# Kernel optimization log

Measured on AMD Instinct MI355X. Metric: run time of the kernel, lower is better.

The kernel has to match this reference:

```python
import jax, jax.numpy as jnp
import numpy as np

B, S, HID = 2, 2048, 4096
H, KV, D = 32, 8, 128
ROPE_BASE = 10000.0
SCALE = 1.0 / (D ** 0.5)


def setup_inputs() -> dict:
    key = jax.random.key(0)
    k1, k2, k3 = jax.random.split(key, 3)
    hidden_states = jax.random.normal(k1, (B, S, HID), dtype=jnp.float32)
    position_ids = jnp.broadcast_to(jnp.arange(S, dtype=jnp.int32)[None, :], (B, S))
    Wqkv = jax.random.normal(k2, ((H + 2 * KV) * D, HID), dtype=jnp.float32) * (HID ** -0.5)
    Wo = jax.random.normal(k3, (HID, HID), dtype=jnp.float32) * (HID ** -0.5)
    return {"hidden_states": hidden_states, "position_ids": position_ids,
            "Wqkv": Wqkv, "Wo": Wo}


def _rotate_half(x):
    x1, x2 = jnp.split(x, 2, axis=-1)
    return jnp.concatenate([-x2, x1], axis=-1)


def _rope_cos_sin(position_ids):
    # inv_freq: [D/2]
    inv_freq = 1.0 / (ROPE_BASE ** (jnp.arange(0, D, 2, dtype=jnp.float32) / D))
    freqs = position_ids.astype(jnp.float32)[:, :, None] * inv_freq[None, None, :]  # [B,S,D/2]
    emb = jnp.concatenate([freqs, freqs], axis=-1)  # [B,S,D]
    # broadcast over heads: [B,1,S,D]
    return jnp.cos(emb)[:, None, :, :], jnp.sin(emb)[:, None, :, :]


def reference(hidden_states, position_ids, Wqkv, Wo):
    # fused QKV projection (no bias)
    qkv = jnp.einsum('bsh,oh->bso', hidden_states, Wqkv)  # [B,S,(H+2KV)*D]
    q, k, v = jnp.split(qkv, [H * D, (H + KV) * D], axis=-1)
    q = q.reshape(B, S, H, D).transpose(0, 2, 1, 3)    # [B,H,S,D]
    k = k.reshape(B, S, KV, D).transpose(0, 2, 1, 3)   # [B,KV,S,D]
    v = v.reshape(B, S, KV, D).transpose(0, 2, 1, 3)   # [B,KV,S,D]

    cos, sin = _rope_cos_sin(position_ids)
    q = q * cos + _rotate_half(q) * sin
    k = k * cos + _rotate_half(k) * sin

    # GQA: repeat_interleave kv heads to match q heads
    rep = H // KV
    k_full = jnp.repeat(k, rep, axis=1)  # [B,H,S,D]
    v_full = jnp.repeat(v, rep, axis=1)

    scores = jnp.einsum('bhqd,bhkd->bhqk', q, k_full) * SCALE  # [B,H,S,S]
    causal = jnp.tril(jnp.ones((S, S), dtype=bool))
    scores = jnp.where(causal[None, None, :, :], scores, jnp.float32(-jnp.inf))
    attn = jax.nn.softmax(scores, axis=-1)
    out = jnp.einsum('bhqk,bhkd->bhqd', attn, v_full)  # [B,H,S,D]
    out = out.transpose(0, 2, 1, 3).reshape(B, S, H * D)
    return jnp.einsum('bso,ho->bsh', out, Wo)  # o_proj, Wo is [out,in]
```

## Files before the change

kernel.cpp:

```cpp
#include <hip/hip_runtime.h>
#include <stdint.h>
#include <stddef.h>

#define Bsz   2
#define Ssz   2048
#define HIDsz 4096
#define Hsz   32
#define KVsz  8
#define Dsz   128
#define NQKV  6144
#define QSCALE 0.12752057463f
#define L2_1E4_64 0.20762050595f

typedef __bf16 bf16x8 __attribute__((ext_vector_type(8)));
typedef __bf16 bf16x2 __attribute__((ext_vector_type(2)));
typedef float  f32x4  __attribute__((ext_vector_type(4)));
typedef float  f32x16 __attribute__((ext_vector_type(16)));
typedef unsigned short u16;
typedef u16 u16x4 __attribute__((ext_vector_type(4)));
typedef u16 u16x8 __attribute__((ext_vector_type(8)));
typedef uint32_t u32x4 __attribute__((ext_vector_type(4)));

__device__ __forceinline__ u16 f2bf(float f) {
  uint32_t u = __builtin_bit_cast(uint32_t, f);
  u = (u + 0x7FFFu + ((u >> 16) & 1u)) >> 16;
  return (u16)u;
}
__device__ __forceinline__ float bf2f(u16 h) {
  return __builtin_bit_cast(float, (uint32_t)h << 16);
}
__device__ __forceinline__ uint32_t packc(float lo, float hi_) {
  bf16x2 t;
  t[0] = (__bf16)lo; t[1] = (__bf16)hi_;
  return __builtin_bit_cast(uint32_t, t);
}

#define GLDS(gp, lp) __builtin_amdgcn_global_load_lds( \
    (__attribute__((address_space(1))) void*)(void*)(gp), \
    (__attribute__((address_space(3))) void*)(lp), 16, 0, 0)

#define N4_HS  ((Bsz * Ssz * HIDsz) / 4)
#define N4_WQ  ((NQKV * HIDsz) / 4)
#define N4_WO  ((HIDsz * HIDsz) / 4)
__global__ __launch_bounds__(256) void k_cvt3(const float* __restrict__ hs,
                                              const float* __restrict__ wqkv,
                                              const float* __restrict__ wo,
                                              u16* __restrict__ xbf,
                                              u16* __restrict__ wqbf,
                                              u16* __restrict__ wobf) {
  int i = blockIdx.x * 256 + threadIdx.x;
  const float* src; u16* dst; int off;
  if (i < N4_HS)                   { src = hs;   dst = xbf;  off = i; }
  else if (i < N4_HS + N4_WQ)      { src = wqkv; dst = wqbf; off = i - N4_HS; }
  else if (i < N4_HS + N4_WQ + N4_WO) { src = wo; dst = wobf; off = i - N4_HS - N4_WQ; }
  else return;
  float4 v = ((const float4*)src)[off];
  u16x4 o;
  o.x = f2bf(v.x); o.y = f2bf(v.y); o.z = f2bf(v.z); o.w = f2bf(v.w);
  ((u16x4*)dst)[off] = o;
}


#define BARX do { asm volatile("" ::: "memory"); __builtin_amdgcn_s_barrier(); \
                  asm volatile("" ::: "memory"); } while (0)
#define VM6  asm volatile("s_waitcnt vmcnt(6)" ::: "memory")
#define VM0  asm volatile("s_waitcnt vmcnt(0)" ::: "memory")

#define LOADA4(P_, Q_, F_) do {                                               \
    afr[F_][0] = LDA(P_, Q_, 0, 0); afr[F_][1] = LDA(P_, Q_, 0, 1);           \
    afr[F_][2] = LDA(P_, Q_, 1, 0); afr[F_][3] = LDA(P_, Q_, 1, 1);           \
  } while (0)

#define LOADB8(P_) do {                                                       \
    _Pragma("unroll") for (int nf = 0; nf < 4; ++nf) {                        \
      bfr[nf][0] = LDB(P_, nf, 0); bfr[nf][1] = LDB(P_, nf, 1); }             \
  } while (0)

#define MMA16(Q_, F_) do {                                                    \
    __builtin_amdgcn_s_setprio(1);                                            \
    _Pragma("unroll") for (int nf = 0; nf < 4; ++nf) {                        \
      acc[(Q_)*2][nf]   = __builtin_amdgcn_mfma_f32_16x16x32_bf16(afr[F_][0], bfr[nf][0], acc[(Q_)*2][nf],   0,0,0); \
      acc[(Q_)*2+1][nf] = __builtin_amdgcn_mfma_f32_16x16x32_bf16(afr[F_][2], bfr[nf][0], acc[(Q_)*2+1][nf], 0,0,0); \
    }                                                                         \
    _Pragma("unroll") for (int nf = 0; nf < 4; ++nf) {                        \
      acc[(Q_)*2][nf]   = __builtin_amdgcn_mfma_f32_16x16x32_bf16(afr[F_][1], bfr[nf][1], acc[(Q_)*2][nf],   0,0,0); \
      acc[(Q_)*2+1][nf] = __builtin_amdgcn_mfma_f32_16x16x32_bf16(afr[F_][3], bfr[nf][1], acc[(Q_)*2+1][nf], 0,0,0); \
    }                                                                         \
    __builtin_amdgcn_s_setprio(0);                                            \
  } while (0)

#define TLS 258

template <int MODE>
__global__ __launch_bounds__(512, 1) void k_gemm256(const u16* __restrict__ A,
                                                    const u16* __restrict__ Bm,
                                                    float* __restrict__ Cv,
                                                    const int* __restrict__ pos,
                                                    u16* __restrict__ Qr,
                                                    u16* __restrict__ Kr,
                                                    u16* __restrict__ Vt,
                                                    int M, int N, int K) {
  constexpr int LDS_BYTES = MODE ? (256 * TLS * 2) : (4 * 256 * 64 * 2);
  __shared__ __align__(16) char LDSBUF[LDS_BYTES];
  u16* SA0 = (u16*)LDSBUF;
  u16* SB0 = (u16*)(LDSBUF + 65536);
  const int tid = threadIdx.x;
  const int w = tid >> 6, lane = tid & 63;
  const int g = lane >> 4, t = lane & 15;
  const int wr = w >> 2, wc = w & 3;
  const int MBt = M >> 8;
  const int cpx = gridDim.x >> 3;
  const int swz = (blockIdx.x & 7) * cpx + (blockIdx.x >> 3);
  const int bm = swz % MBt, bn = swz / MBt;
  const int m0 = bm << 8, n0 = bn << 8;

  const char* Ab = (const char*)A;
  const char* Bb = (const char*)Bm;
  const size_t rowK = (size_t)K * 2;
  const int srcx = ((lane & 7) ^ (lane >> 3)) << 4;
  const int l3 = lane >> 3;
  const int tx = (t & 7) << 4;

  auto SToff = [&](int h, int j) -> int {
    int ii = w * 2 + j;
    return (ii < 8) ? (h * 64 + ii * 8) : (128 + h * 64 + (ii - 8) * 8);
  };
  auto STAGE_A = [&](int p, int T, int h) {
#pragma unroll
    for (int j = 0; j < 2; ++j) {
      int rb = SToff(h, j);
      GLDS(Ab + (size_t)(m0 + rb + l3) * rowK + (size_t)T * 128 + srcx,
           &SA0[p * 16384 + rb * 64]);
    }
  };
  auto STAGE_B = [&](int p, int T, int h) {
#pragma unroll
    for (int j = 0; j < 2; ++j) {
      int rb = SToff(h, j);
      GLDS(Bb + (size_t)(n0 + rb + l3) * rowK + (size_t)T * 128 + srcx,
           &SB0[p * 16384 + rb * 64]);
    }
  };
  auto LDA = [&](int p, int q, int fr, int kk) -> bf16x8 {
    int ar = wr * 128 + q * 32 + fr * 16 + t;
    const char* ptr = (const char*)&SA0[p * 16384] + ar * 128 + ((kk * 64 + 16 * g) ^ tx);
    return __builtin_bit_cast(bf16x8, *(const u16x8*)ptr);
  };
  auto LDB = [&](int p, int nf, int kk) -> bf16x8 {
    int br = wc * 64 + nf * 16 + t;
    const char* ptr = (const char*)&SB0[p * 16384] + br * 128 + ((kk * 64 + 16 * g) ^ tx);
    return __builtin_bit_cast(bf16x8, *(const u16x8*)ptr);
  };

  f32x4 acc[8][4];
#pragma unroll
  for (int i = 0; i < 8; ++i)
#pragma unroll
    for (int j = 0; j < 4; ++j) acc[i][j] = (f32x4){0.f, 0.f, 0.f, 0.f};
  bf16x8 bfr[4][2];
  bf16x8 afr[2][4];

  STAGE_A(0, 0, 0); STAGE_B(0, 0, 0); STAGE_A(0, 0, 1); STAGE_B(0, 0, 1);
  STAGE_A(1, 1, 0); STAGE_B(1, 1, 0); STAGE_B(1, 1, 1);
  VM6;
  __builtin_amdgcn_s_barrier();

  const int NI = (K >> 7) - 1;
  for (int i = 0; i < NI; ++i) {
    const int T1 = 2 * i + 1, T2 = 2 * i + 2, T3 = 2 * i + 3;
    LOADB8(0); LOADA4(0, 0, 0);
    STAGE_A(1, T1, 1); LOADA4(0, 1, 1); MMA16(0, 0); BARX;
    STAGE_B(0, T2, 0); LOADA4(0, 2, 0); MMA16(1, 1); BARX;
    STAGE_B(0, T2, 1); LOADA4(0, 3, 1); MMA16(2, 0); BARX;
    STAGE_A(0, T2, 0); MMA16(3, 1); VM6; BARX;
    LOADB8(1); LOADA4(1, 0, 0);
    STAGE_A(0, T2, 1); LOADA4(1, 1, 1); MMA16(0, 0); BARX;
    STAGE_B(1, T3, 0); LOADA4(1, 2, 0); MMA16(1, 1); BARX;
    STAGE_A(1, T3, 0); LOADA4(1, 3, 1); MMA16(2, 0); BARX;
    STAGE_B(1, T3, 1); MMA16(3, 1); VM6; BARX;
  }
  {
    const int TL_ = (K >> 6) - 1;
    LOADB8(0); LOADA4(0, 0, 0);
    STAGE_A(1, TL_, 1); LOADA4(0, 1, 1); MMA16(0, 0); BARX;
    LOADA4(0, 2, 0); MMA16(1, 1); BARX;
    LOADA4(0, 3, 1); MMA16(2, 0); BARX;
    MMA16(3, 1); VM0; BARX;
    LOADB8(1); LOADA4(1, 0, 0);
    LOADA4(1, 1, 1); MMA16(0, 0); BARX;
    LOADA4(1, 2, 0); MMA16(1, 1); BARX;
    LOADA4(1, 3, 1); MMA16(2, 0); BARX;
    MMA16(3, 1);
  }

  if constexpr (MODE == 0) {
#pragma unroll
    for (int fi = 0; fi < 8; ++fi)
#pragma unroll
      for (int nf = 0; nf < 4; ++nf)
#pragma unroll
        for (int r = 0; r < 4; ++r) {
          int row = m0 + wr * 128 + fi * 16 + 4 * g + r;
          int col = n0 + wc * 64 + nf * 16 + t;
          Cv[(size_t)row * N + col] = acc[fi][nf][r];
        }
  } else {
    u16* TL = (u16*)LDSBUF;
    __syncthreads();
#pragma unroll
    for (int fi = 0; fi < 8; ++fi)
#pragma unroll
      for (int nf = 0; nf < 4; ++nf)
#pragma unroll
        for (int r = 0; r < 4; ++r)
          TL[(wr * 128 + fi * 16 + 4 * g + r) * TLS + wc * 64 + nf * 16 + t] =
              f2bf(acc[fi][nf][r]);
    __syncthreads();

    if (n0 < (Hsz + KVsz) * Dsz) {
      const bool isQ = (n0 < Hsz * Dsz);
      const int j = lane;
      const float ifr = exp2f(-(float)j * L2_1E4_64);
#pragma unroll 1
      for (int it = 0; it < 64; ++it) {
        int combo = w * 64 + it;
        int row = combo & 255;
        int hh = combo >> 8;
        int tok = m0 + row;
        int b = tok >> 11, s = tok & (Ssz - 1);
        float x1 = bf2f(TL[row * TLS + hh * 128 + j]);
        float x2 = bf2f(TL[row * TLS + hh * 128 + 64 + j]);
        float p = (float)pos[tok];
        float ang = p * ifr;
        float sn, cs;
        __sincosf(ang, &sn, &cs);
        float o1 = x1 * cs - x2 * sn;
        float o2 = x2 * cs + x1 * sn;
        u16* o;
        if (isQ) {
          int h = (n0 >> 7) + hh;
          o = Qr + ((size_t)(b * Hsz + h) * Ssz + s) * Dsz;
          o1 *= QSCALE; o2 *= QSCALE;
        } else {
          int kvh = ((n0 - Hsz * Dsz) >> 7) + hh;
          o = Kr + ((size_t)(b * KVsz + kvh) * Ssz + s) * Dsz;
        }
        o[j] = f2bf(o1); o[j + 64] = f2bf(o2);
      }
    } else {
      const int dbase = n0 - (Hsz + KVsz) * Dsz;
#pragma unroll 1
      for (int it = 0; it < 32; ++it) {
        int col = w * 32 + it;
        int dg = dbase + col;
        int kvh = dg >> 7, d = dg & 127;
        int tok0 = m0 + 4 * lane;
        int b = tok0 >> 11, s0 = tok0 & (Ssz - 1);
        u16x4 v4;
#pragma unroll
        for (int i2 = 0; i2 < 4; ++i2)
          v4[i2] = TL[(4 * lane + i2) * TLS + col];
        *(u16x4*)(Vt + ((size_t)(b * KVsz + kvh) * Dsz + d) * Ssz + s0) = v4;
      }
    }
  }
}

__global__ __launch_bounds__(512, 1) void k_attn(const u16* __restrict__ Qr,
                                                 const u16* __restrict__ Kr,
                                                 const u16* __restrict__ Vt,
                                                 u16* __restrict__ AO) {
  __shared__ __align__(16) u16 Kl[2][64 * 128];
  __shared__ __align__(16) u16 Vl[2][128 * 64];
  const int tid = threadIdx.x;
  const int w = tid >> 6, lane = tid & 63;
  const int q = lane & 31, hi = lane >> 5;
  const int bh = blockIdx.y;
  const int b = bh >> 5, h = bh & 31;
  const int kvh = h >> 2;
  const int bxr = gridDim.x - 1 - blockIdx.x;
  const int q0 = bxr * 256;
  const int qw = q0 + w * 32;
  const int ntiles = 4 * bxr + 4;
  const int qg = qw + q;

  const u16* Qb = Qr + ((size_t)bh * Ssz + qw + q) * Dsz + hi * 8;
  bf16x8 qf[8];
#pragma unroll
  for (int ds = 0; ds < 8; ++ds)
    qf[ds] = __builtin_bit_cast(bf16x8, *(const u16x8*)(Qb + ds * 16));

  f32x16 oacc[4];
#pragma unroll
  for (int dt = 0; dt < 4; ++dt)
#pragma unroll
    for (int r = 0; r < 16; ++r) oacc[dt][r] = 0.f;
  float mr = -1e30f, lr = 0.f;

  const int xq = (q & 7) << 4;
  int koff[8][2], voff[4][4];
#pragma unroll
  for (int ds = 0; ds < 8; ++ds) {
    int c = (ds * 32 + hi * 16) ^ xq;
    koff[ds][0] = q * 256 + c;
    koff[ds][1] = (32 + q) * 256 + c;
  }
#pragma unroll
  for (int ks = 0; ks < 4; ++ks) {
    int c = (ks * 32 + hi * 16) ^ xq;
#pragma unroll
    for (int dt = 0; dt < 4; ++dt)
      voff[ks][dt] = (dt * 32 + q) * 128 + c;
  }

  const char* Kbase = (const char*)(Kr + (size_t)(b * KVsz + kvh) * Ssz * Dsz);
  const char* Vbase = (const char*)(Vt + (size_t)(b * KVsz + kvh) * Dsz * Ssz);

  auto STAGE = [&](int bu, int kt2) {
    const char* Kb = Kbase + (size_t)kt2 * (64 * 256);
    const char* Vb = Vbase + (size_t)kt2 * 128;
#pragma unroll
    for (int j = 0; j < 2; ++j) {
      int flat = j * 512 + tid;
      int row = flat >> 4, colb = ((flat & 15) * 16) ^ ((row & 7) << 4);
      GLDS(Kb + (size_t)row * 256 + colb, (char*)&Kl[bu][0] + flat * 16);
    }
#pragma unroll
    for (int j = 0; j < 2; ++j) {
      int flat = j * 512 + tid;
      int row = flat >> 3, colb = ((flat & 7) * 16) ^ ((row & 7) << 4);
      GLDS(Vb + (size_t)row * (Ssz * 2) + colb, (char*)&Vl[bu][0] + flat * 16);
    }
  };

  STAGE(0, 0);
  __syncthreads();

  auto TILE = [&](int bufc, int kt) {
    const int k0 = kt * 64;
    if (kt + 1 < ntiles) STAGE(bufc ^ 1, kt + 1);

    if (k0 <= qw + 31) {
      const char* Kb = (const char*)&Kl[bufc][0];
      const char* Vb = (const char*)&Vl[bufc][0];
      f32x16 pa0, pa1;
#pragma unroll
      for (int r = 0; r < 16; ++r) { pa0[r] = 0.f; pa1[r] = 0.f; }
      __builtin_amdgcn_s_setprio(1);
#pragma unroll
      for (int ds = 0; ds < 8; ++ds) {
        bf16x8 kf0 = __builtin_bit_cast(bf16x8, *(const u16x8*)(Kb + koff[ds][0]));
        pa0 = __builtin_amdgcn_mfma_f32_32x32x16_bf16(kf0, qf[ds], pa0, 0, 0, 0);
        bf16x8 kf1 = __builtin_bit_cast(bf16x8, *(const u16x8*)(Kb + koff[ds][1]));
        pa1 = __builtin_amdgcn_mfma_f32_32x32x16_bf16(kf1, qf[ds], pa1, 0, 0, 0);
      }
      __builtin_amdgcn_s_setprio(0);

      if (k0 + 63 > qw) {
#pragma unroll
        for (int reg = 0; reg < 16; ++reg) {
          const int kb = (reg & 3) + 8 * (reg >> 2) + 4 * hi;
          if (k0 + kb > qg)      pa0[reg] = -1e30f;
          if (k0 + 32 + kb > qg) pa1[reg] = -1e30f;
        }
      }
      float tmx[16];
#pragma unroll
      for (int i = 0; i < 16; ++i) tmx[i] = fmaxf(pa0[i], pa1[i]);
#pragma unroll
      for (int s = 8; s > 0; s >>= 1)
#pragma unroll
        for (int i = 0; i < s; ++i) tmx[i] = fmaxf(tmx[i], tmx[i + s]);
      const float mx = fmaxf(tmx[0], __shfl_xor(tmx[0], 32, 64));
      if (!__all(mx <= mr + 4.0f)) {
        const float mnew = fmaxf(mr, mx);
        const float corr = exp2f(mr - mnew);
        lr *= corr;
#pragma unroll
        for (int dt = 0; dt < 4; ++dt)
#pragma unroll
          for (int reg = 0; reg < 16; ++reg) oacc[dt][reg] *= corr;
        mr = mnew;
      }
      float su[16];
#pragma unroll
      for (int reg = 0; reg < 16; ++reg) {
        pa0[reg] = exp2f(pa0[reg] - mr);
        pa1[reg] = exp2f(pa1[reg] - mr);
        su[reg] = pa0[reg] + pa1[reg];
      }
#pragma unroll
      for (int s = 8; s > 0; s >>= 1)
#pragma unroll
        for (int i = 0; i < s; ++i) su[i] += su[i + s];
      lr += su[0] + __shfl_xor(su[0], 32, 64);

      uint32_t W0[4][2], W1[4][2];
#pragma unroll
      for (int r2 = 0; r2 < 4; ++r2)
#pragma unroll
        for (int c = 0; c < 2; ++c) {
          W0[r2][c] = packc(pa0[4 * r2 + 2 * c], pa0[4 * r2 + 2 * c + 1]);
          W1[r2][c] = packc(pa1[4 * r2 + 2 * c], pa1[4 * r2 + 2 * c + 1]);
        }

      __builtin_amdgcn_s_setprio(1);
#pragma unroll
      for (int ks = 0; ks < 4; ++ks) {
        const int T = ks >> 1, r2e = 2 * (ks & 1);
        uint32_t a0 = T ? W1[r2e][0]     : W0[r2e][0];
        uint32_t a1 = T ? W1[r2e][1]     : W0[r2e][1];
        uint32_t b0 = T ? W1[r2e + 1][0] : W0[r2e + 1][0];
        uint32_t b1 = T ? W1[r2e + 1][1] : W0[r2e + 1][1];
        asm("v_permlane32_swap_b32 %0, %1" : "+v"(a0), "+v"(b0));
        asm("v_permlane32_swap_b32 %0, %1" : "+v"(a1), "+v"(b1));
        u32x4 fw; fw[0] = a0; fw[1] = a1; fw[2] = b0; fw[3] = b1;
        bf16x8 pf = __builtin_bit_cast(bf16x8, fw);
#pragma unroll
        for (int dt = 0; dt < 4; ++dt) {
          bf16x8 vf = __builtin_bit_cast(bf16x8, *(const u16x8*)(Vb + voff[ks][dt]));
          oacc[dt] = __builtin_amdgcn_mfma_f32_32x32x16_bf16(vf, pf, oacc[dt], 0, 0, 0);
        }
      }
      __builtin_amdgcn_s_setprio(0);
    }
    __syncthreads();
  };

  for (int kt = 0; kt < ntiles; kt += 2) {
    TILE(0, kt);
    TILE(1, kt + 1);
  }

  const float inv = 1.f / lr;
  u16* Ob = AO + ((size_t)(b * Ssz) + qw + q) * HIDsz + h * Dsz + hi * 4;
#pragma unroll
  for (int dt = 0; dt < 4; ++dt)
#pragma unroll
    for (int r2 = 0; r2 < 4; ++r2) {
      u16x4 o4;
#pragma unroll
      for (int j = 0; j < 4; ++j) o4[j] = f2bf(oacc[dt][4 * r2 + j] * inv);
      *(u16x4*)(Ob + dt * 32 + r2 * 8) = o4;
    }
}

extern "C" void kernel_launch(void* const* d_in, const int* in_sizes, int n_in,
                              void* d_out, int out_size, void* d_ws, size_t ws_size,
                              hipStream_t stream) {
  (void)in_sizes; (void)n_in; (void)out_size;
  const float* hs   = (const float*)d_in[0];
  const int*   pos  = (const int*)d_in[1];
  const float* Wqkv = (const float*)d_in[2];
  const float* Wo   = (const float*)d_in[3];

  char* ws = (char*)d_ws;
  const size_t SZ_XBF = (size_t)4096 * 4096 * 2;
  const size_t SZ_WQ  = (size_t)6144 * 4096 * 2;
  const size_t SZ_WO  = (size_t)4096 * 4096 * 2;
  const size_t SZ_QR  = (size_t)Bsz * Hsz * Ssz * Dsz * 2;
  const size_t SZ_KR  = (size_t)Bsz * KVsz * Ssz * Dsz * 2;
  const size_t SZ_VT  = SZ_KR;

  size_t off = 0;
  u16*   Xbf   = (u16*)(ws + off);  off += SZ_XBF;
  u16*   Wq_bf = (u16*)(ws + off);  off += SZ_WQ;
  u16*   Wo_bf = (u16*)(ws + off);  off += SZ_WO;
  u16*   Qr    = (u16*)(ws + off);  off += SZ_QR;
  u16*   Kr    = (u16*)(ws + off);  off += SZ_KR;
  u16*   Vt    = (u16*)(ws + off);  off += SZ_VT;
  u16*   AO    = Xbf;
  if (ws_size < off) return;

  k_cvt3<<<(N4_HS + N4_WQ + N4_WO + 255) / 256, 256, 0, stream>>>(
      hs, Wqkv, Wo, Xbf, Wq_bf, Wo_bf);

  k_gemm256<1><<<dim3((NQKV / 256) * ((Bsz * Ssz) / 256)), 512, 0, stream>>>(
      Xbf, Wq_bf, nullptr, pos, Qr, Kr, Vt, Bsz * Ssz, NQKV, HIDsz);

  k_attn<<<dim3(Ssz / 256, Bsz * Hsz), 512, 0, stream>>>(Qr, Kr, Vt, AO);

  k_gemm256<0><<<dim3((HIDsz / 256) * ((Bsz * Ssz) / 256)), 512, 0, stream>>>(
      AO, Wo_bf, (float*)d_out, nullptr, nullptr, nullptr, nullptr,
      Bsz * Ssz, HIDsz, HIDsz);
}
```

Before: 541.6 us.

## Split QKV GEMM into Q tiles plus split-K KV tiles with separate epilogues

```diff
diff --git a/kernel.cpp b/kernel.cpp
--- a/kernel.cpp
+++ b/kernel.cpp
@@ -97,10 +97,9 @@
                                                     float* __restrict__ Cv,
                                                     const int* __restrict__ pos,
                                                     u16* __restrict__ Qr,
-                                                    u16* __restrict__ Kr,
-                                                    u16* __restrict__ Vt,
-                                                    int M, int N, int K) {
-  constexpr int LDS_BYTES = MODE ? (256 * TLS * 2) : (4 * 256 * 64 * 2);
+                                                    int M, int N, int K_ld,
+                                                    int K_len) {
+  constexpr int LDS_BYTES = (MODE == 1) ? (256 * TLS * 2) : (4 * 256 * 64 * 2);
   __shared__ __align__(16) char LDSBUF[LDS_BYTES];
   u16* SA0 = (u16*)LDSBUF;
   u16* SB0 = (u16*)(LDSBUF + 65536);
@@ -108,15 +107,26 @@
   const int w = tid >> 6, lane = tid & 63;
   const int g = lane >> 4, t = lane & 15;
   const int wr = w >> 2, wc = w & 3;
-  const int MBt = M >> 8;
   const int cpx = gridDim.x >> 3;
   const int swz = (blockIdx.x & 7) * cpx + (blockIdx.x >> 3);
-  const int bm = swz % MBt, bn = swz / MBt;
+
+  int bm, bn;
+  const u16 *Au = A, *Bu = Bm;
+  float* Cu = Cv;
+  if constexpr (MODE == 2) {
+    const int t2 = swz & 127, h2 = swz >> 7;
+    bm = t2 & 15; bn = 16 + (t2 >> 4);
+    Au = A + h2 * 2048; Bu = Bm + h2 * 2048;
+    Cu = Cv + (size_t)h2 * 4096 * 2048;
+  } else {
+    const int MBt = M >> 8;
+    bm = swz % MBt; bn = swz / MBt;
+  }
   const int m0 = bm << 8, n0 = bn << 8;
 
-  const char* Ab = (const char*)A;
-  const char* Bb = (const char*)Bm;
-  const size_t rowK = (size_t)K * 2;
+  const char* Ab = (const char*)Au;
+  const char* Bb = (const char*)Bu;
+  const size_t rowK = (size_t)K_ld * 2;
   const int srcx = ((lane & 7) ^ (lane >> 3)) << 4;
   const int l3 = lane >> 3;
   const int tx = (t & 7) << 4;
@@ -165,7 +175,7 @@
   VM6;
   __builtin_amdgcn_s_barrier();
 
-  const int NI = (K >> 7) - 1;
+  const int NI = (K_len >> 7) - 1;
   for (int i = 0; i < NI; ++i) {
     const int T1 = 2 * i + 1, T2 = 2 * i + 2, T3 = 2 * i + 3;
     LOADB8(0); LOADA4(0, 0, 0);
@@ -180,7 +190,7 @@
     STAGE_B(1, T3, 1); MMA16(3, 1); VM6; BARX;
   }
   {
-    const int TL_ = (K >> 6) - 1;
+    const int TL_ = (K_len >> 6) - 1;
     LOADB8(0); LOADA4(0, 0, 0);
     STAGE_A(1, TL_, 1); LOADA4(0, 1, 1); MMA16(0, 0); BARX;
     LOADA4(0, 2, 0); MMA16(1, 1); BARX;
@@ -193,7 +203,9 @@
     MMA16(3, 1);
   }
 
-  if constexpr (MODE == 0) {
+  if constexpr (MODE == 0 || MODE == 2) {
+    const int cstride = (MODE == 0) ? N : 2048;
+    const int cbase   = (MODE == 0) ? n0 : (n0 - 4096);
 #pragma unroll
     for (int fi = 0; fi < 8; ++fi)
 #pragma unroll
@@ -201,8 +213,8 @@
 #pragma unroll
         for (int r = 0; r < 4; ++r) {
           int row = m0 + wr * 128 + fi * 16 + 4 * g + r;
-          int col = n0 + wc * 64 + nf * 16 + t;
-          Cv[(size_t)row * N + col] = acc[fi][nf][r];
+          int col = cbase + wc * 64 + nf * 16 + t;
+          Cu[(size_t)row * cstride + col] = acc[fi][nf][r];
         }
   } else {
     u16* TL = (u16*)LDSBUF;
@@ -217,52 +229,85 @@
               f2bf(acc[fi][nf][r]);
     __syncthreads();
 
-    if (n0 < (Hsz + KVsz) * Dsz) {
-      const bool isQ = (n0 < Hsz * Dsz);
-      const int j = lane;
-      const float ifr = exp2f(-(float)j * L2_1E4_64);
+    const int j = lane;
+    const float ifr = exp2f(-(float)j * L2_1E4_64);
 #pragma unroll 1
-      for (int it = 0; it < 64; ++it) {
-        int combo = w * 64 + it;
-        int row = combo & 255;
-        int hh = combo >> 8;
-        int tok = m0 + row;
-        int b = tok >> 11, s = tok & (Ssz - 1);
-        float x1 = bf2f(TL[row * TLS + hh * 128 + j]);
-        float x2 = bf2f(TL[row * TLS + hh * 128 + 64 + j]);
-        float p = (float)pos[tok];
-        float ang = p * ifr;
-        float sn, cs;
-        __sincosf(ang, &sn, &cs);
-        float o1 = x1 * cs - x2 * sn;
-        float o2 = x2 * cs + x1 * sn;
-        u16* o;
-        if (isQ) {
-          int h = (n0 >> 7) + hh;
-          o = Qr + ((size_t)(b * Hsz + h) * Ssz + s) * Dsz;
-          o1 *= QSCALE; o2 *= QSCALE;
-        } else {
-          int kvh = ((n0 - Hsz * Dsz) >> 7) + hh;
-          o = Kr + ((size_t)(b * KVsz + kvh) * Ssz + s) * Dsz;
-        }
-        o[j] = f2bf(o1); o[j + 64] = f2bf(o2);
-      }
-    } else {
-      const int dbase = n0 - (Hsz + KVsz) * Dsz;
-#pragma unroll 1
-      for (int it = 0; it < 32; ++it) {
-        int col = w * 32 + it;
-        int dg = dbase + col;
-        int kvh = dg >> 7, d = dg & 127;
-        int tok0 = m0 + 4 * lane;
-        int b = tok0 >> 11, s0 = tok0 & (Ssz - 1);
-        u16x4 v4;
-#pragma unroll
-        for (int i2 = 0; i2 < 4; ++i2)
-          v4[i2] = TL[(4 * lane + i2) * TLS + col];
-        *(u16x4*)(Vt + ((size_t)(b * KVsz + kvh) * Dsz + d) * Ssz + s0) = v4;
-      }
-    }
+    for (int it = 0; it < 64; ++it) {
+      int combo = w * 64 + it;
+      int row = combo & 255;
+      int hh = combo >> 8;
+      int tok = m0 + row;
+      int b = tok >> 11, s = tok & (Ssz - 1);
+      float x1 = bf2f(TL[row * TLS + hh * 128 + j]);
+      float x2 = bf2f(TL[row * TLS + hh * 128 + 64 + j]);
+      float p = (float)pos[tok];
+      float ang = p * ifr;
+      float sn, cs;
+      __sincosf(ang, &sn, &cs);
+      float o1 = (x1 * cs - x2 * sn) * QSCALE;
+      float o2 = (x2 * cs + x1 * sn) * QSCALE;
+      int h = (n0 >> 7) + hh;
+      u16* o = Qr + ((size_t)(b * Hsz + h) * Ssz + s) * Dsz;
+      o[j] = f2bf(o1); o[j + 64] = f2bf(o2);
+    }
+  }
+}
+
+__global__ __launch_bounds__(256) void k_ropeK2(const float* __restrict__ Cp,
+                                                const int* __restrict__ pos,
+                                                u16* __restrict__ Kr) {
+  int idx = blockIdx.x * 256 + threadIdx.x;
+  if (idx >= Bsz * Ssz * KVsz * 64) return;
+  const size_t OFF2 = (size_t)4096 * 2048;
+  int j = idx & 63;
+  int kvh = (idx >> 6) & 7;
+  int bs = idx >> 9;
+  size_t p0 = (size_t)bs * 2048 + kvh * 128 + j;
+  float x1 = Cp[p0] + Cp[p0 + OFF2];
+  float x2 = Cp[p0 + 64] + Cp[p0 + 64 + OFF2];
+  float p = (float)pos[bs];
+  float ang = p * exp2f(-(float)j * L2_1E4_64);
+  float sn, cs;
+  __sincosf(ang, &sn, &cs);
+  int b = bs >> 11, sidx = bs & (Ssz - 1);
+  u16* o = Kr + ((size_t)(b * KVsz + kvh) * Ssz + sidx) * Dsz;
+  o[j] = f2bf(x1 * cs - x2 * sn);
+  o[j + 64] = f2bf(x2 * cs + x1 * sn);
+}
+
+__global__ __launch_bounds__(256) void k_vtrans2(const float* __restrict__ Cp,
+                                                 u16* __restrict__ Vt) {
+  __shared__ __align__(16) u16 Tl[64 * 72];
+  const int tid = threadIdx.x;
+  const int bk = blockIdx.y;
+  const int s0 = (blockIdx.x >> 1) * 64;
+  const int d0 = (blockIdx.x & 1) * 64;
+  const int b = bk >> 3, kvh = bk & 7;
+  const size_t OFF2 = (size_t)4096 * 2048;
+  const size_t base = (size_t)(b * Ssz + s0) * 2048 + 1024 + kvh * 128 + d0;
+#pragma unroll
+  for (int p = 0; p < 2; ++p) {
+    int cid = p * 256 + tid;
+    int r = cid >> 3, co = cid & 7;
+    int chunk = co ^ ((r >> 3) & 7);
+    const float* s1 = Cp + base + (size_t)r * 2048 + co * 8;
+    u16x8 v;
+#pragma unroll
+    for (int e = 0; e < 8; ++e) v[e] = f2bf(s1[e] + s1[OFF2 + e]);
+    *(u16x8*)((char*)Tl + r * 144 + chunk * 16) = v;
+  }
+  __syncthreads();
+#pragma unroll
+  for (int p = 0; p < 2; ++p) {
+    int cid = p * 256 + tid;
+    int dr = cid >> 3, c = cid & 7;
+    u16x8 v;
+#pragma unroll
+    for (int j = 0; j < 8; ++j) {
+      int s = 8 * c + j;
+      v[j] = *(const u16*)((char*)Tl + s * 144 + (((dr >> 3) ^ c) * 16) + (dr & 7) * 2);
+    }
+    *(u16x8*)(Vt + ((size_t)bk * Dsz + d0 + dr) * Ssz + s0 + 8 * c) = v;
   }
 }
 
@@ -470,17 +515,23 @@
   u16*   Kr    = (u16*)(ws + off);  off += SZ_KR;
   u16*   Vt    = (u16*)(ws + off);  off += SZ_VT;
   u16*   AO    = Xbf;
+  float* Cp    = (float*)d_out;
   if (ws_size < off) return;
 
   k_cvt3<<<(N4_HS + N4_WQ + N4_WO + 255) / 256, 256, 0, stream>>>(
       hs, Wqkv, Wo, Xbf, Wq_bf, Wo_bf);
 
-  k_gemm256<1><<<dim3((NQKV / 256) * ((Bsz * Ssz) / 256)), 512, 0, stream>>>(
-      Xbf, Wq_bf, nullptr, pos, Qr, Kr, Vt, Bsz * Ssz, NQKV, HIDsz);
+  k_gemm256<1><<<256, 512, 0, stream>>>(Xbf, Wq_bf, nullptr, pos, Qr,
+                                        Bsz * Ssz, NQKV, HIDsz, HIDsz);
+
+  k_gemm256<2><<<256, 512, 0, stream>>>(Xbf, Wq_bf, Cp, nullptr, nullptr,
+                                        Bsz * Ssz, NQKV, HIDsz, 2048);
+
+  k_ropeK2<<<(Bsz * Ssz * KVsz * 64) / 256, 256, 0, stream>>>(Cp, pos, Kr);
+  k_vtrans2<<<dim3(64, Bsz * KVsz), 256, 0, stream>>>(Cp, Vt);
 
   k_attn<<<dim3(Ssz / 256, Bsz * Hsz), 512, 0, stream>>>(Qr, Kr, Vt, AO);
 
-  k_gemm256<0><<<dim3((HIDsz / 256) * ((Bsz * Ssz) / 256)), 512, 0, stream>>>(
-      AO, Wo_bf, (float*)d_out, nullptr, nullptr, nullptr, nullptr,
-      Bsz * Ssz, HIDsz, HIDsz);
-}
+  k_gemm256<0><<<256, 512, 0, stream>>>(AO, Wo_bf, (float*)d_out, nullptr,
+                                        nullptr, Bsz * Ssz, HIDsz, HIDsz, HIDsz);
+}
```

Result: faster. 526.7 us (-2.8%).
